# Kernel tuning notes

Hardware: AMD Instinct MI355X
Metric: run time of the kernel (lower is better)

The kernel has to match this reference:

```python
import jax, jax.numpy as jnp
import numpy as np

N, IN, OUT, F = 8192, 128, 128, 2
P_EDGE = 0.004  # ~32 neighbors per row


def _sparse_lap(k1, k2):
    mask = jax.random.uniform(k1, (N, N)) < P_EDGE
    mask = mask | jnp.eye(N, dtype=bool)  # nonzero diagonal, like a Laplacian
    vals = jax.random.normal(k2, (N, N), dtype=jnp.float32)
    return jnp.where(mask, vals, 0.0)


def setup_inputs() -> dict:
    key = jax.random.key(0)
    ks = jax.random.split(key, 11)
    x = jax.random.normal(ks[0], (N, IN), dtype=jnp.float32)
    lap_up = _sparse_lap(ks[1], ks[2])
    lap_down = _sparse_lap(ks[3], ks[4])
    proj = jax.random.normal(ks[5], (N, N), dtype=jnp.float32) * np.float32(1.0 / np.sqrt(N))
    scale = np.float32(1.0 / np.sqrt(IN))
    W_up = jax.random.normal(ks[6], (F, IN, OUT), dtype=jnp.float32) * scale
    W_down = jax.random.normal(ks[7], (F, IN, OUT), dtype=jnp.float32) * scale
    a_up = jax.random.normal(ks[8], (2 * OUT * F,), dtype=jnp.float32) * np.float32(0.1)
    a_down = jax.random.normal(ks[9], (2 * OUT * F,), dtype=jnp.float32) * np.float32(0.1)
    W_har = jax.random.normal(ks[10], (IN, OUT), dtype=jnp.float32) * scale
    return dict(x=x, laplacian_up=lap_up, laplacian_down=lap_down, projection_mat=proj,
                W_up=W_up, a_up=a_up, W_down=W_down, a_down=a_down, W_har=W_har)


def _san_conv(x, neighborhood, W, a):
    # W: [F, in, out]; a: [2*out*F]
    n = x.shape[0]
    f, _, out = W.shape
    z = jnp.einsum('ni,fio->fno', x, W)                      # [F, N, out] (x @ weight)
    z_r = jnp.transpose(z, (1, 0, 2)).reshape(n, f * out)    # permute(1,0,2).reshape
    a_src, a_tgt = a[: f * out], a[f * out:]                 # cat([source_j, target_i]) @ a
    s = z_r @ a_src                                          # [N] per-source term
    t = z_r @ a_tgt                                          # [N] per-target term
    mask = neighborhood != 0                                 # sparse pattern of laplacian
    logits = jnp.where(mask, jax.nn.elu(t[:, None] + s[None, :]), -jnp.inf)
    att = jnp.where(mask, jax.nn.softmax(logits, axis=1), 0.0)  # sparse softmax over dim=1
    # sum_{p=1}^{F} att^p @ z[p-1]
    out_msg = jnp.zeros((n, out), dtype=x.dtype)
    A = att
    for p in range(f):
        out_msg = out_msg + A @ z[p]
        if p + 1 < f:
            A = A @ att
    return out_msg


def reference(x, laplacian_up, laplacian_down, projection_mat, W_up, a_up, W_down, a_down, W_har):
    z_down = _san_conv(x, laplacian_down, W_down, a_down)
    z_up = _san_conv(x, laplacian_up, W_up, a_up)
    z_har = projection_mat @ (x @ W_har)
    return z_down + z_up + z_har
```

## Files before the change

kernel.cpp:

```cpp
#include <hip/hip_runtime.h>

#define NN 8192
#define CAP 128

typedef __attribute__((ext_vector_type(8))) short bf16x8;
typedef __attribute__((ext_vector_type(4))) float f32x4;

__device__ __forceinline__ short f2bf(float f) {
    unsigned u = __builtin_bit_cast(unsigned, f);
    u += 0x7FFFu + ((u >> 16) & 1u);
    return (short)(u >> 16);
}

__global__ __launch_bounds__(256) void k_small_gemm(
        const float* __restrict__ x, const float* __restrict__ Wdown,
        const float* __restrict__ Wup, const float* __restrict__ Whar,
        float* __restrict__ zbuf) {
    int wsel = blockIdx.y;
    const float* W = (wsel == 0) ? Wdown : (wsel == 1) ? Wdown + 16384 :
                     (wsel == 2) ? Wup   : (wsel == 3) ? Wup + 16384 : Whar;
    float* out = zbuf + (size_t)wsel * NN * 128;
    __shared__ float Wl[128 * 128];
    __shared__ float Xl[32 * 128];
    int tid = threadIdx.x;
    int row0 = blockIdx.x * 32;
    const float4* W4 = (const float4*)W;
    float4* Wl4 = (float4*)Wl;
    for (int i = tid; i < 4096; i += 256) Wl4[i] = W4[i];
    const float4* X4 = (const float4*)(x + (size_t)row0 * 128);
    float4* Xl4 = (float4*)Xl;
    for (int i = tid; i < 1024; i += 256) Xl4[i] = X4[i];
    __syncthreads();
    int tx = tid & 31, ty = tid >> 5;
    float acc[4][4] = {};
#pragma unroll 2
    for (int i = 0; i < 128; ++i) {
        float w0 = Wl[i * 128 + tx];
        float w1 = Wl[i * 128 + tx + 32];
        float w2 = Wl[i * 128 + tx + 64];
        float w3 = Wl[i * 128 + tx + 96];
#pragma unroll
        for (int rr = 0; rr < 4; ++rr) {
            float xv = Xl[(ty * 4 + rr) * 128 + i];
            acc[rr][0] += xv * w0; acc[rr][1] += xv * w1;
            acc[rr][2] += xv * w2; acc[rr][3] += xv * w3;
        }
    }
#pragma unroll
    for (int rr = 0; rr < 4; ++rr) {
        float* o = out + (size_t)(row0 + ty * 4 + rr) * 128 + tx;
        o[0] = acc[rr][0]; o[32] = acc[rr][1]; o[64] = acc[rr][2]; o[96] = acc[rr][3];
    }
}

__global__ __launch_bounds__(256) void k_st(
        const float* __restrict__ zbuf, const float* __restrict__ a_down,
        const float* __restrict__ a_up, float* __restrict__ stbuf) {
    int sel = blockIdx.y;
    const float* z0 = zbuf + (size_t)sel * 2 * NN * 128;
    const float* z1 = z0 + (size_t)NN * 128;
    const float* a = sel ? a_up : a_down;
    int row = ((int)blockIdx.x * 256 + (int)threadIdx.x) >> 6;
    int lane = threadIdx.x & 63;
    float z0a = z0[(size_t)row * 128 + lane], z0b = z0[(size_t)row * 128 + lane + 64];
    float z1a = z1[(size_t)row * 128 + lane], z1b = z1[(size_t)row * 128 + lane + 64];
    float ps = z0a * a[lane]       + z0b * a[lane + 64]
             + z1a * a[128 + lane] + z1b * a[192 + lane];
    float pt = z0a * a[256 + lane] + z0b * a[320 + lane]
             + z1a * a[384 + lane] + z1b * a[448 + lane];
    for (int off = 32; off; off >>= 1) {
        ps += __shfl_xor(ps, off);
        pt += __shfl_xor(pt, off);
    }
    if (lane == 0) {
        stbuf[(size_t)sel * 2 * NN + row] = ps;
        stbuf[(size_t)sel * 2 * NN + NN + row] = pt;
    }
}

__global__ __launch_bounds__(256) void k_scan(
        const float* __restrict__ lapdown, const float* __restrict__ lapup,
        int* __restrict__ cntbuf, int* __restrict__ colbuf) {
    int sel = blockIdx.y;
    const float* lap = sel ? lapup : lapdown;
    int row = ((int)blockIdx.x * 256 + (int)threadIdx.x) >> 6;
    int lane = threadIdx.x & 63;
    const float4* lr = (const float4*)(lap + (size_t)row * NN);
    int* crow = colbuf + (size_t)sel * NN * CAP + (size_t)row * CAP;
    unsigned long long ltmask = (1ull << lane) - 1ull;
    int c = 0;
    for (int it = 0; it < 32; ++it) {
        float4 v = lr[it * 64 + lane];
#pragma unroll
        for (int q = 0; q < 4; ++q) {
            float f = (q == 0) ? v.x : (q == 1) ? v.y : (q == 2) ? v.z : v.w;
            bool nz = (f != 0.0f);
            unsigned long long m = __ballot(nz);
            if (nz) {
                int slot = c + __popcll(m & ltmask);
                if (slot < CAP) crow[slot] = it * 256 + lane * 4 + q;
            }
            c += __popcll(m);
        }
    }
    if (lane == 0) cntbuf[sel * NN + row] = (c < CAP) ? c : CAP;
}

__global__ __launch_bounds__(256) void k_att(
        const float* __restrict__ stbuf, const int* __restrict__ cntbuf,
        const int* __restrict__ colbuf, float* __restrict__ valbuf) {
    int sel = blockIdx.y;
    const float* s = stbuf + (size_t)sel * 2 * NN;
    const float* t = s + NN;
    int row = ((int)blockIdx.x * 256 + (int)threadIdx.x) >> 6;
    int lane = threadIdx.x & 63;
    int c = cntbuf[sel * NN + row];
    const int* cr = colbuf + (size_t)sel * NN * CAP + (size_t)row * CAP;
    float* vr = valbuf + (size_t)sel * NN * CAP + (size_t)row * CAP;
    float tv = t[row];
    float e0 = -1e30f, e1 = -1e30f;
    if (lane < c)      { float v = tv + s[cr[lane]];      e0 = v > 0.f ? v : expm1f(v); }
    if (lane + 64 < c) { float v = tv + s[cr[lane + 64]]; e1 = v > 0.f ? v : expm1f(v); }
    float m = fmaxf(e0, e1);
    for (int off = 32; off; off >>= 1) m = fmaxf(m, __shfl_xor(m, off));
    float p0 = (lane < c)      ? expf(e0 - m) : 0.f;
    float p1 = (lane + 64 < c) ? expf(e1 - m) : 0.f;
    float sum = p0 + p1;
    for (int off = 32; off; off >>= 1) sum += __shfl_xor(sum, off);
    float inv = 1.0f / sum;
    if (lane < c)      vr[lane] = p0 * inv;
    if (lane + 64 < c) vr[lane + 64] = p1 * inv;
}

__global__ __launch_bounds__(512) void k_tr(
        const float* __restrict__ h, unsigned short* __restrict__ hT) {
    __shared__ unsigned short tile[32 * 128];
    int tid = threadIdx.x;
    int k0 = blockIdx.x * 32;
    int r = tid >> 4;
    int c0 = (tid & 15) * 8;
    const float4* src = (const float4*)(h + (size_t)(k0 + r) * 128 + c0);
    float4 a = src[0], b = src[1];
    unsigned short* tp = &tile[r * 128 + c0];
    tp[0] = (unsigned short)f2bf(a.x); tp[1] = (unsigned short)f2bf(a.y);
    tp[2] = (unsigned short)f2bf(a.z); tp[3] = (unsigned short)f2bf(a.w);
    tp[4] = (unsigned short)f2bf(b.x); tp[5] = (unsigned short)f2bf(b.y);
    tp[6] = (unsigned short)f2bf(b.z); tp[7] = (unsigned short)f2bf(b.w);
    __syncthreads();
    int c = tid & 127;
    int seg = tid >> 7;
    unsigned short v[8];
#pragma unroll
    for (int i = 0; i < 8; ++i) v[i] = tile[(seg * 8 + i) * 128 + c];
    uint4 pack;
    pack.x = (unsigned)v[0] | ((unsigned)v[1] << 16);
    pack.y = (unsigned)v[2] | ((unsigned)v[3] << 16);
    pack.z = (unsigned)v[4] | ((unsigned)v[5] << 16);
    pack.w = (unsigned)v[6] | ((unsigned)v[7] << 16);
    *(uint4*)(hT + (size_t)c * NN + k0 + seg * 8) = pack;
}

__global__ __launch_bounds__(256) void k_proj(
        const float* __restrict__ P, const unsigned short* __restrict__ hT,
        float* __restrict__ partial) {
    int gw = ((int)blockIdx.x * 256 + (int)threadIdx.x) >> 6;
    int lane = threadIdx.x & 63;
    int strip = gw >> 3;
    int ks = gw & 7;
    int row0 = strip * 16;
    int k0 = ks * 1024;
    int l15 = lane & 15;
    int koff = (lane >> 4) * 8;
    const float* A = P + (size_t)(row0 + l15) * NN + k0 + koff;
    const unsigned short* B0 = hT + (size_t)l15 * NN + k0 + koff;
    f32x4 acc[8];
#pragma unroll
    for (int i = 0; i < 8; ++i) acc[i] = (f32x4){0.f, 0.f, 0.f, 0.f};
#pragma unroll 2
    for (int kc = 0; kc < 32; ++kc) {
        int k = kc * 32;
        float4 a0 = *(const float4*)(A + k);
        float4 a1 = *(const float4*)(A + k + 4);
        bf16x8 af;
        af[0] = f2bf(a0.x); af[1] = f2bf(a0.y); af[2] = f2bf(a0.z); af[3] = f2bf(a0.w);
        af[4] = f2bf(a1.x); af[5] = f2bf(a1.y); af[6] = f2bf(a1.z); af[7] = f2bf(a1.w);
#pragma unroll
        for (int ct = 0; ct < 8; ++ct) {
            bf16x8 bf = *(const bf16x8*)(B0 + (size_t)ct * 16 * NN + k);
            acc[ct] = __builtin_amdgcn_mfma_f32_16x16x32_bf16(af, bf, acc[ct], 0, 0, 0);
        }
    }
    float* out = partial + (size_t)ks * NN * 128;
    int prow = row0 + (lane >> 4) * 4;
#pragma unroll
    for (int ct = 0; ct < 8; ++ct)
#pragma unroll
        for (int r = 0; r < 4; ++r)
            out[(size_t)(prow + r) * 128 + ct * 16 + l15] = acc[ct][r];
}

__global__ __launch_bounds__(256) void k_reduce(
        const float4* __restrict__ partial, float4* __restrict__ out) {
    int i = blockIdx.x * 256 + threadIdx.x;
    float4 s = partial[i];
#pragma unroll
    for (int ks = 1; ks < 8; ++ks) {
        float4 p = partial[(size_t)ks * 262144 + i];
        s.x += p.x; s.y += p.y; s.z += p.z; s.w += p.w;
    }
    out[i] = s;
}

__global__ __launch_bounds__(256) void k_spmm(
        const int* __restrict__ cnt, const int* __restrict__ col,
        const float* __restrict__ val, const float* __restrict__ B1,
        const float* __restrict__ B2, float* __restrict__ out, int accumulate) {
    int row = ((int)blockIdx.x * 256 + (int)threadIdx.x) >> 6;
    int lane = threadIdx.x & 63;
    int c = cnt[row];
    const int* cr = col + (size_t)row * CAP;
    const float* vr = val + (size_t)row * CAP;
    float ax = 0.f, ay = 0.f;
    for (int e = 0; e < c; ++e) {
        int j = cr[e];
        float v = vr[e];
        float2 b = ((const float2*)(B1 + (size_t)j * 128))[lane];
        if (B2) {
            float2 b2 = ((const float2*)(B2 + (size_t)j * 128))[lane];
            b.x += b2.x; b.y += b2.y;
        }
        ax += v * b.x; ay += v * b.y;
    }
    float2* o = (float2*)(out + (size_t)row * 128);
    float2 rres;
    if (accumulate) { float2 p = o[lane]; rres.x = p.x + ax; rres.y = p.y + ay; }
    else            { rres.x = ax; rres.y = ay; }
    o[lane] = rres;
}

extern "C" void kernel_launch(void* const* d_in, const int* in_sizes, int n_in,
                              void* d_out, int out_size, void* d_ws, size_t ws_size,
                              hipStream_t stream) {
    const float* x        = (const float*)d_in[0];
    const float* lap_up   = (const float*)d_in[1];
    const float* lap_down = (const float*)d_in[2];
    const float* proj     = (const float*)d_in[3];
    const float* W_up     = (const float*)d_in[4];
    const float* a_up     = (const float*)d_in[5];
    const float* W_down   = (const float*)d_in[6];
    const float* a_down   = (const float*)d_in[7];
    const float* W_har    = (const float*)d_in[8];
    float* out = (float*)d_out;
    float* ws = (float*)d_ws;

    const size_t ZSZ = (size_t)NN * 128;
    size_t off = 0;
    float* zbuf = ws + off;              off += 5 * ZSZ;
    float* stbuf = ws + off;             off += 4 * NN;
    int* cntbuf = (int*)(ws + off);      off += 2 * NN;
    int* colbuf = (int*)(ws + off);      off += 2 * (size_t)NN * CAP;
    float* valbuf = ws + off;            off += 2 * (size_t)NN * CAP;
    float* y1 = ws + off;                off += ZSZ;
    unsigned short* hT = (unsigned short*)(ws + off); off += ZSZ / 2;
    float* partial = ws + off;           off += 8 * ZSZ;

    hipLaunchKernelGGL(k_small_gemm, dim3(256, 5), dim3(256), 0, stream,
                       x, W_down, W_up, W_har, zbuf);
    hipLaunchKernelGGL(k_st, dim3(2048, 2), dim3(256), 0, stream,
                       zbuf, a_down, a_up, stbuf);
    hipLaunchKernelGGL(k_scan, dim3(2048, 2), dim3(256), 0, stream,
                       lap_down, lap_up, cntbuf, colbuf);
    hipLaunchKernelGGL(k_att, dim3(2048, 2), dim3(256), 0, stream,
                       stbuf, cntbuf, colbuf, valbuf);
    hipLaunchKernelGGL(k_tr, dim3(256), dim3(512), 0, stream,
                       zbuf + 4 * ZSZ, hT);
    hipLaunchKernelGGL(k_proj, dim3(1024), dim3(256), 0, stream,
                       proj, hT, partial);
    hipLaunchKernelGGL(k_reduce, dim3(1024), dim3(256), 0, stream,
                       (const float4*)partial, (float4*)out);
    hipLaunchKernelGGL(k_spmm, dim3(2048), dim3(256), 0, stream,
                       cntbuf, colbuf, valbuf, zbuf + ZSZ, (const float*)nullptr, y1, 0);
    hipLaunchKernelGGL(k_spmm, dim3(2048), dim3(256), 0, stream,
                       cntbuf, colbuf, valbuf, zbuf, y1, out, 1);
    hipLaunchKernelGGL(k_spmm, dim3(2048), dim3(256), 0, stream,
                       cntbuf + NN, colbuf + (size_t)NN * CAP, valbuf + (size_t)NN * CAP,
                       zbuf + 3 * ZSZ, (const float*)nullptr, y1, 0);
    hipLaunchKernelGGL(k_spmm, dim3(2048), dim3(256), 0, stream,
                       cntbuf + NN, colbuf + (size_t)NN * CAP, valbuf + (size_t)NN * CAP,
                       zbuf + 2 * ZSZ, y1, out, 1);
}
```

Measured before the change: 974.9 us.

## Refactor sparse message passing via associativity, fuse reduction, unroll SpMM, retune projection split

Rewrites att@z0 + att@(att@z1) as att@(z0 + att@z1). This lets one pass per Laplacian build w, and a single final kernel applies both attention matrices while also summing the projection partials. The separate reduce kernel and four SpMM launches are dropped, and each SpMM inner loop now handles 8 edges per iteration with vector index/value loads, using rows padded with zero entries. The projection GEMM now splits K into a variable number of slices chosen from the workspace size and register-prefetches the next A tile. Risks are more partial buffers to sum in the final kernel and extra padding writes.

```diff
diff --git a/kernel.cpp b/kernel.cpp
--- a/kernel.cpp
+++ b/kernel.cpp
@@ -103,7 +103,10 @@
             c += __popcll(m);
         }
     }
-    if (lane == 0) cntbuf[sel * NN + row] = (c < CAP) ? c : CAP;
+    int cc = (c < CAP) ? c : CAP;
+    int cpad = (cc + 7) & ~7;
+    if (lane < cpad - cc) crow[cc + lane] = 0;
+    if (lane == 0) cntbuf[sel * NN + row] = cc;
 }
 
 __global__ __launch_bounds__(256) void k_att(
@@ -130,6 +133,8 @@
     float inv = 1.0f / sum;
     if (lane < c)      vr[lane] = p0 * inv;
     if (lane + 64 < c) vr[lane + 64] = p1 * inv;
+    int cpad = (c + 7) & ~7;
+    if (lane < cpad - c) vr[c + lane] = 0.f;
 }
 
 __global__ __launch_bounds__(512) void k_tr(
@@ -162,13 +167,15 @@
 
 __global__ __launch_bounds__(256) void k_proj(
         const float* __restrict__ P, const unsigned short* __restrict__ hT,
-        float* __restrict__ partial) {
+        float* __restrict__ partial, int lgnks) {
     int gw = ((int)blockIdx.x * 256 + (int)threadIdx.x) >> 6;
     int lane = threadIdx.x & 63;
-    int strip = gw >> 3;
-    int ks = gw & 7;
+    int nksm1 = (1 << lgnks) - 1;
+    int strip = gw >> lgnks;
+    int ks = gw & nksm1;
+    int kiters = 256 >> lgnks;
     int row0 = strip * 16;
-    int k0 = ks * 1024;
+    int k0 = ks << (13 - lgnks);
     int l15 = lane & 15;
     int koff = (lane >> 4) * 8;
     const float* A = P + (size_t)(row0 + l15) * NN + k0 + koff;
@@ -176,19 +183,25 @@
     f32x4 acc[8];
 #pragma unroll
     for (int i = 0; i < 8; ++i) acc[i] = (f32x4){0.f, 0.f, 0.f, 0.f};
-#pragma unroll 2
-    for (int kc = 0; kc < 32; ++kc) {
-        int k = kc * 32;
-        float4 a0 = *(const float4*)(A + k);
-        float4 a1 = *(const float4*)(A + k + 4);
+    float4 a0 = *(const float4*)(A);
+    float4 a1 = *(const float4*)(A + 4);
+    for (int kc = 0; kc < kiters; ++kc) {
+        float4 n0, n1;
+        if (kc + 1 < kiters) {
+            const float* An = A + 32 * (kc + 1);
+            n0 = *(const float4*)(An);
+            n1 = *(const float4*)(An + 4);
+        }
         bf16x8 af;
         af[0] = f2bf(a0.x); af[1] = f2bf(a0.y); af[2] = f2bf(a0.z); af[3] = f2bf(a0.w);
         af[4] = f2bf(a1.x); af[5] = f2bf(a1.y); af[6] = f2bf(a1.z); af[7] = f2bf(a1.w);
+        const unsigned short* Bp = B0 + kc * 32;
 #pragma unroll
         for (int ct = 0; ct < 8; ++ct) {
-            bf16x8 bf = *(const bf16x8*)(B0 + (size_t)ct * 16 * NN + k);
+            bf16x8 bf = *(const bf16x8*)(Bp + (size_t)ct * 16 * NN);
             acc[ct] = __builtin_amdgcn_mfma_f32_16x16x32_bf16(af, bf, acc[ct], 0, 0, 0);
         }
+        a0 = n0; a1 = n1;
     }
     float* out = partial + (size_t)ks * NN * 128;
     int prow = row0 + (lane >> 4) * 4;
@@ -199,43 +212,68 @@
             out[(size_t)(prow + r) * 128 + ct * 16 + l15] = acc[ct][r];
 }
 
-__global__ __launch_bounds__(256) void k_reduce(
-        const float4* __restrict__ partial, float4* __restrict__ out) {
-    int i = blockIdx.x * 256 + threadIdx.x;
-    float4 s = partial[i];
-#pragma unroll
-    for (int ks = 1; ks < 8; ++ks) {
-        float4 p = partial[(size_t)ks * 262144 + i];
-        s.x += p.x; s.y += p.y; s.z += p.z; s.w += p.w;
-    }
-    out[i] = s;
-}
-
-__global__ __launch_bounds__(256) void k_spmm(
+__device__ __forceinline__ void edge_acc(
+        int c, const int* __restrict__ cr, const float* __restrict__ vr,
+        const float* __restrict__ B, int lane, float& ax, float& ay) {
+    int cpad = (c + 7) & ~7;
+    for (int e = 0; e < cpad; e += 8) {
+        int4   j0 = *(const int4*)(cr + e);
+        int4   j1 = *(const int4*)(cr + e + 4);
+        float4 v0 = *(const float4*)(vr + e);
+        float4 v1 = *(const float4*)(vr + e + 4);
+        float2 b0 = ((const float2*)(B + (size_t)j0.x * 128))[lane];
+        float2 b1 = ((const float2*)(B + (size_t)j0.y * 128))[lane];
+        float2 b2 = ((const float2*)(B + (size_t)j0.z * 128))[lane];
+        float2 b3 = ((const float2*)(B + (size_t)j0.w * 128))[lane];
+        float2 b4 = ((const float2*)(B + (size_t)j1.x * 128))[lane];
+        float2 b5 = ((const float2*)(B + (size_t)j1.y * 128))[lane];
+        float2 b6 = ((const float2*)(B + (size_t)j1.z * 128))[lane];
+        float2 b7 = ((const float2*)(B + (size_t)j1.w * 128))[lane];
+        ax += v0.x * b0.x; ay += v0.x * b0.y;
+        ax += v0.y * b1.x; ay += v0.y * b1.y;
+        ax += v0.z * b2.x; ay += v0.z * b2.y;
+        ax += v0.w * b3.x; ay += v0.w * b3.y;
+        ax += v1.x * b4.x; ay += v1.x * b4.y;
+        ax += v1.y * b5.x; ay += v1.y * b5.y;
+        ax += v1.z * b6.x; ay += v1.z * b6.y;
+        ax += v1.w * b7.x; ay += v1.w * b7.y;
+    }
+}
+
+__global__ __launch_bounds__(256) void k_pass1(
         const int* __restrict__ cnt, const int* __restrict__ col,
-        const float* __restrict__ val, const float* __restrict__ B1,
-        const float* __restrict__ B2, float* __restrict__ out, int accumulate) {
-    int row = ((int)blockIdx.x * 256 + (int)threadIdx.x) >> 6;
-    int lane = threadIdx.x & 63;
-    int c = cnt[row];
-    const int* cr = col + (size_t)row * CAP;
-    const float* vr = val + (size_t)row * CAP;
+        const float* __restrict__ val, const float* __restrict__ zbuf,
+        float* __restrict__ wbuf) {
+    int sel = blockIdx.y;
+    const float* z0 = zbuf + (size_t)sel * 2 * NN * 128;
+    const float* z1 = z0 + (size_t)NN * 128;
+    float* w = wbuf + (size_t)sel * NN * 128;
+    int row = ((int)blockIdx.x * 256 + (int)threadIdx.x) >> 6;
+    int lane = threadIdx.x & 63;
+    int c = cnt[sel * NN + row];
+    float2 a = ((const float2*)(z0 + (size_t)row * 128))[lane];
+    float ax = a.x, ay = a.y;
+    edge_acc(c, col + ((size_t)sel * NN + row) * CAP,
+             val + ((size_t)sel * NN + row) * CAP, z1, lane, ax, ay);
+    ((float2*)(w + (size_t)row * 128))[lane] = make_float2(ax, ay);
+}
+
+__global__ __launch_bounds__(256) void k_final(
+        const int* __restrict__ cnt, const int* __restrict__ col,
+        const float* __restrict__ val, const float* __restrict__ wbuf,
+        const float* __restrict__ partial, int nks, float* __restrict__ out) {
+    int row = ((int)blockIdx.x * 256 + (int)threadIdx.x) >> 6;
+    int lane = threadIdx.x & 63;
     float ax = 0.f, ay = 0.f;
-    for (int e = 0; e < c; ++e) {
-        int j = cr[e];
-        float v = vr[e];
-        float2 b = ((const float2*)(B1 + (size_t)j * 128))[lane];
-        if (B2) {
-            float2 b2 = ((const float2*)(B2 + (size_t)j * 128))[lane];
-            b.x += b2.x; b.y += b2.y;
-        }
-        ax += v * b.x; ay += v * b.y;
-    }
-    float2* o = (float2*)(out + (size_t)row * 128);
-    float2 rres;
-    if (accumulate) { float2 p = o[lane]; rres.x = p.x + ax; rres.y = p.y + ay; }
-    else            { rres.x = ax; rres.y = ay; }
-    o[lane] = rres;
+    for (int ks = 0; ks < nks; ++ks) {
+        float2 p = ((const float2*)(partial + (size_t)ks * NN * 128 + (size_t)row * 128))[lane];
+        ax += p.x; ay += p.y;
+    }
+    edge_acc(cnt[row], col + (size_t)row * CAP, val + (size_t)row * CAP,
+             wbuf, lane, ax, ay);
+    edge_acc(cnt[NN + row], col + ((size_t)NN + row) * CAP,
+             val + ((size_t)NN + row) * CAP, wbuf + (size_t)NN * 128, lane, ax, ay);
+    ((float2*)(out + (size_t)row * 128))[lane] = make_float2(ax, ay);
 }
 
 extern "C" void kernel_launch(void* const* d_in, const int* in_sizes, int n_in,
@@ -254,15 +292,21 @@
     float* ws = (float*)d_ws;
 
     const size_t ZSZ = (size_t)NN * 128;
+    const size_t fixed = 5 * ZSZ + 4 * NN + 2 * NN + 2 * ZSZ + 2 * ZSZ
+                       + 2 * ZSZ + ZSZ / 2;
+    int lgnks = 4;
+    while (lgnks > 2 && (fixed + ((size_t)1 << lgnks) * ZSZ) * 4 > ws_size) --lgnks;
+    int nks = 1 << lgnks;
+
     size_t off = 0;
     float* zbuf = ws + off;              off += 5 * ZSZ;
     float* stbuf = ws + off;             off += 4 * NN;
     int* cntbuf = (int*)(ws + off);      off += 2 * NN;
-    int* colbuf = (int*)(ws + off);      off += 2 * (size_t)NN * CAP;
-    float* valbuf = ws + off;            off += 2 * (size_t)NN * CAP;
-    float* y1 = ws + off;                off += ZSZ;
+    int* colbuf = (int*)(ws + off);      off += 2 * ZSZ;
+    float* valbuf = ws + off;            off += 2 * ZSZ;
+    float* wbuf = ws + off;              off += 2 * ZSZ;
     unsigned short* hT = (unsigned short*)(ws + off); off += ZSZ / 2;
-    float* partial = ws + off;           off += 8 * ZSZ;
+    float* partial = ws + off;           off += (size_t)nks * ZSZ;
 
     hipLaunchKernelGGL(k_small_gemm, dim3(256, 5), dim3(256), 0, stream,
                        x, W_down, W_up, W_har, zbuf);
@@ -274,18 +318,10 @@
                        stbuf, cntbuf, colbuf, valbuf);
     hipLaunchKernelGGL(k_tr, dim3(256), dim3(512), 0, stream,
                        zbuf + 4 * ZSZ, hT);
-    hipLaunchKernelGGL(k_proj, dim3(1024), dim3(256), 0, stream,
-                       proj, hT, partial);
-    hipLaunchKernelGGL(k_reduce, dim3(1024), dim3(256), 0, stream,
-                       (const float4*)partial, (float4*)out);
-    hipLaunchKernelGGL(k_spmm, dim3(2048), dim3(256), 0, stream,
-                       cntbuf, colbuf, valbuf, zbuf + ZSZ, (const float*)nullptr, y1, 0);
-    hipLaunchKernelGGL(k_spmm, dim3(2048), dim3(256), 0, stream,
-                       cntbuf, colbuf, valbuf, zbuf, y1, out, 1);
-    hipLaunchKernelGGL(k_spmm, dim3(2048), dim3(256), 0, stream,
-                       cntbuf + NN, colbuf + (size_t)NN * CAP, valbuf + (size_t)NN * CAP,
-                       zbuf + 3 * ZSZ, (const float*)nullptr, y1, 0);
-    hipLaunchKernelGGL(k_spmm, dim3(2048), dim3(256), 0, stream,
-                       cntbuf + NN, colbuf + (size_t)NN * CAP, valbuf + (size_t)NN * CAP,
-                       zbuf + 2 * ZSZ, y1, out, 1);
-}
+    hipLaunchKernelGGL(k_proj, dim3(128 * nks), dim3(256), 0, stream,
+                       proj, hT, partial, lgnks);
+    hipLaunchKernelGGL(k_pass1, dim3(2048, 2), dim3(256), 0, stream,
+                       cntbuf, colbuf, valbuf, zbuf, wbuf);
+    hipLaunchKernelGGL(k_final, dim3(2048), dim3(256), 0, stream,
+                       cntbuf, colbuf, valbuf, wbuf, partial, nks, out);
+}
```

Result: faster. 936.5 us (-3.9%).
